# Kernel optimization log

Hardware: AMD Instinct MI355X
Metric: run time of the kernel (lower is better)

Reference implementation:

```python
import jax, jax.numpy as jnp
import numpy as np
import math

B, NX, NY = 8, 1024, 1024
DIM_X = DIM_Y = DIM = 1024
H = 8


def layer_norm(x, g, b, eps=1e-5):
    mu = jnp.mean(x, axis=-1, keepdims=True)
    var = jnp.mean(jnp.square(x - mu), axis=-1, keepdims=True)
    return (x - mu) * jax.lax.rsqrt(var + eps) * g + b


def setup_inputs() -> dict:
    key = jax.random.key(0)
    ks = jax.random.split(key, 12)
    s = 1.0 / math.sqrt(DIM)
    return {
        "X": jax.random.normal(ks[0], (B, NX, DIM_X), jnp.float32),
        "Y": jax.random.normal(ks[1], (B, NY, DIM_Y), jnp.float32),
        "mask": jax.random.bernoulli(ks[2], 0.1, (B, NY)),  # True = masked out
        "Wq": jax.random.normal(ks[3], (DIM_X, DIM), jnp.float32) * s,
        "bq": jnp.zeros((DIM,), jnp.float32),
        "Wk": jax.random.normal(ks[4], (DIM_Y, DIM), jnp.float32) * s,
        "bk": jnp.zeros((DIM,), jnp.float32),
        "Wv": jax.random.normal(ks[5], (DIM_Y, DIM), jnp.float32) * s,
        "bv": jnp.zeros((DIM,), jnp.float32),
        "Wo": jax.random.normal(ks[6], (DIM, DIM), jnp.float32) * s,
        "bo": jnp.zeros((DIM,), jnp.float32),
        "g1": jnp.ones((DIM,), jnp.float32),
        "b1": jnp.zeros((DIM,), jnp.float32),
        "g2": jnp.ones((DIM,), jnp.float32),
        "b2": jnp.zeros((DIM,), jnp.float32),
    }


def reference(X, Y, mask, Wq, bq, Wk, bk, Wv, bv, Wo, bo, g1, b1, g2, b2):
    Q = X @ Wq + bq            # [B, NX, DIM]
    K = Y @ Wk + bk            # [B, NY, DIM]
    V = Y @ Wv + bv            # [B, NY, DIM]
    Dh = DIM // H
    Qh = Q.reshape(B, NX, H, Dh)
    Kh = K.reshape(B, NY, H, Dh)
    Vh = V.reshape(B, NY, H, Dh)
    # NOTE: original scales by sqrt(dim) (full model dim), not sqrt(head_dim)
    logits = jnp.einsum("bqhd,bkhd->bhqk", Qh, Kh) / math.sqrt(DIM)
    logits = jnp.where(mask[:, None, None, :], -jnp.inf, logits)
    A = jax.nn.softmax(logits, axis=-1)
    A = jnp.where(jnp.isnan(A), 0.0, A)  # fully-masked rows -> 0
    attn = jnp.einsum("bhqk,bkhd->bqhd", A, Vh).reshape(B, NX, DIM)
    O = layer_norm(Q + attn, g1, b1)
    O = layer_norm(O + jax.nn.relu(O @ Wo + bo), g2, b2)
    return O
```

## Files before the change

### kernel.cpp

```cpp
#include <hip/hip_runtime.h>
#include <stdint.h>


typedef unsigned short u16;
typedef unsigned int u32;
typedef __attribute__((ext_vector_type(8))) short s16x8;
typedef __attribute__((ext_vector_type(4))) float f32x4;
typedef __attribute__((ext_vector_type(16))) float f32x16;
typedef __attribute__((ext_vector_type(4))) u16 u16x4;
typedef __attribute__((ext_vector_type(4))) u32 u32x4;

typedef __attribute__((address_space(1))) const void* as1cv;
typedef __attribute__((address_space(3))) void* as3v;

#define DEVINL __device__ __forceinline__

DEVINL u16 f2bf(float f) {
  union { float f; u32 u; } v; v.f = f;
  return (u16)((v.u + 0x7FFFu + ((v.u >> 16) & 1u)) >> 16);
}
DEVINL float bf2f(u16 x) {
  union { u32 u; float f; } v; v.u = ((u32)x) << 16;
  return v.f;
}
DEVINL u32 cvtpk_bf16(float lo, float hi) {
  u32 r;
  asm("v_cvt_pk_bf16_f32 %0, %1, %2" : "=v"(r) : "v"(lo), "v"(hi));
  return r;
}
DEVINL float fexp2(float x) {
  float r;
  asm("v_exp_f32 %0, %1" : "=v"(r) : "v"(x));
  return r;
}
DEVINL void gload_lds16(const void* g, void* l) {
  __builtin_amdgcn_global_load_lds((as1cv)g, (as3v)l, 16, 0, 0);
}
DEVINL f32x4 mfma16(s16x8 a, s16x8 b, f32x4 c) {
  return __builtin_amdgcn_mfma_f32_16x16x32_bf16(a, b, c, 0, 0, 0);
}
DEVINL f32x16 mfma32(s16x8 a, s16x8 b, f32x16 c) {
  return __builtin_amdgcn_mfma_f32_32x32x16_bf16(a, b, c, 0, 0, 0);
}
template <int N> DEVINL void wait_vm() {
  asm volatile("s_waitcnt vmcnt(%0)" :: "i"(N) : "memory");
  __builtin_amdgcn_sched_barrier(0);
}
DEVINL void wait_lgkm0() {
  asm volatile("s_waitcnt lgkmcnt(0)" ::: "memory");
  __builtin_amdgcn_sched_barrier(0);
}
DEVINL void barrier_raw() {
  __builtin_amdgcn_sched_barrier(0);
  __builtin_amdgcn_s_barrier();
  __builtin_amdgcn_sched_barrier(0);
}

__global__ __launch_bounds__(256) void prep_all(
    const float* __restrict__ X, u16* __restrict__ Xbf,
    const float* __restrict__ Y, u16* __restrict__ Ybf,
    const float* __restrict__ W0, const float* __restrict__ W1,
    const float* __restrict__ W2, const float* __restrict__ W3,
    u16* __restrict__ T0, u16* __restrict__ T1,
    u16* __restrict__ T2, u16* __restrict__ T3,
    const u32* __restrict__ mraw, float* __restrict__ maskb) {
  const int bid = blockIdx.x;
  const int t = threadIdx.x;
  if (bid < 2048) {
    const int base = bid * 256 + t;
#pragma unroll
    for (int k = 0; k < 4; ++k) {
      int e0 = (base + k * 524288) * 2;
      const float* in = X;
      u16* out = Xbf;
      if (e0 >= 2097152) { e0 -= 2097152; in = Y; out = Ybf; }
      float4 v0 = *(const float4*)(in + (size_t)e0 * 4);
      float4 v1 = *(const float4*)(in + (size_t)e0 * 4 + 4);
      u32x4 o;
      o[0] = cvtpk_bf16(v0.x, v0.y);
      o[1] = cvtpk_bf16(v0.z, v0.w);
      o[2] = cvtpk_bf16(v1.x, v1.y);
      o[3] = cvtpk_bf16(v1.z, v1.w);
      *(u32x4*)(out + (size_t)e0 * 4) = o;
    }
    return;
  }
  if (bid < 6144) {
    const int r = bid - 2048;
    const int z = r >> 10, tile = r & 1023;
    const int bx = tile & 31, by = tile >> 5;
    const float* W = (z == 0) ? W0 : (z == 1) ? W1 : (z == 2) ? W2 : W3;
    u16* T = (z == 0) ? T0 : (z == 1) ? T1 : (z == 2) ? T2 : T3;
    __shared__ float tl[32][33];
    const int tx = t & 31, ty = t >> 5;
    const int N0 = bx << 5, K0 = by << 5;
#pragma unroll
    for (int i = 0; i < 4; ++i)
      tl[ty + i * 8][tx] = W[(size_t)(K0 + ty + i * 8) * 1024 + N0 + tx];
    __syncthreads();
#pragma unroll
    for (int i = 0; i < 4; ++i)
      T[(size_t)(N0 + ty + i * 8) * 1024 + K0 + tx] = f2bf(tl[tx][ty + i * 8]);
    return;
  }
  __shared__ int mode;
  int fB = 0, fF = 0;
  for (int i = t; i < 2048; i += 256) {
    u32 v = mraw[i];
    if (v == 0x3F800000u) fF = 1;
    else if (v > 1u) fB = 1;
  }
  if (t == 0) mode = 0;
  __syncthreads();
  if (fB) atomicOr(&mode, 1);
  if (fF) atomicOr(&mode, 2);
  __syncthreads();
  const int md = mode;
  const int idx = (bid - 6144) * 256 + t;
  int v;
  if (md & 1)       v = ((const unsigned char*)mraw)[idx] != 0;
  else if (md & 2)  v = ((const float*)mraw)[idx] != 0.0f;
  else              v = ((const int*)mraw)[idx] != 0;
  maskb[idx] = v ? -3e30f : -11.54156032f;
}

#define GEMM_KLOOP                                                            \
  for (int kt = 0; kt < 16; ++kt) {                                           \
    s16x8 af0[4], bf0[4], af1[4], bf1[4];                                     \
    _Pragma("unroll")                                                         \
    for (int mi = 0; mi < 4; ++mi) {                                          \
      int row = wm * 64 + mi * 16 + lrow;                                     \
      int off = row * 128 + ((lk * 16) ^ ((row & 7) << 4));                   \
      af0[mi] = *(const s16x8*)((const char*)lA + off);                       \
    }                                                                         \
    _Pragma("unroll")                                                         \
    for (int ni = 0; ni < 4; ++ni) {                                          \
      int row = wn * 64 + ni * 16 + lrow;                                     \
      int off = row * 128 + ((lk * 16) ^ ((row & 7) << 4));                   \
      bf0[ni] = *(const s16x8*)((const char*)lB + off);                       \
    }                                                                         \
    _Pragma("unroll")                                                         \
    for (int mi = 0; mi < 4; ++mi)                                            \
      _Pragma("unroll")                                                       \
      for (int ni = 0; ni < 4; ++ni)                                          \
        acc[mi][ni] = mfma16(af0[mi], bf0[ni], acc[mi][ni]);                  \
    _Pragma("unroll")                                                         \
    for (int mi = 0; mi < 4; ++mi) {                                          \
      int row = wm * 64 + mi * 16 + lrow;                                     \
      int off = row * 128 + ((lk * 16 + 64) ^ ((row & 7) << 4));              \
      af1[mi] = *(const s16x8*)((const char*)lA + off);                       \
    }                                                                         \
    _Pragma("unroll")                                                         \
    for (int ni = 0; ni < 4; ++ni) {                                          \
      int row = wn * 64 + ni * 16 + lrow;                                     \
      int off = row * 128 + ((lk * 16 + 64) ^ ((row & 7) << 4));              \
      bf1[ni] = *(const s16x8*)((const char*)lB + off);                       \
    }                                                                         \
    wait_lgkm0();                                                             \
    barrier_raw();                                                            \
    if (kt < 15) {                                                            \
      const int kb = (kt + 1) * 128;                                          \
      _Pragma("unroll")                                                       \
      for (int c = 0; c < 4; ++c) {                                           \
        int row = (w * 4 + c) * 8 + sr;                                       \
        gload_lds16(gA + (size_t)row * 2048 + kb + scol,                      \
                    (char*)lA + (w * 4 + c) * 1024);                          \
        gload_lds16(gB + (size_t)row * 2048 + kb + scol,                      \
                    (char*)lB + (w * 4 + c) * 1024);                          \
      }                                                                       \
    }                                                                         \
    _Pragma("unroll")                                                         \
    for (int mi = 0; mi < 4; ++mi)                                            \
      _Pragma("unroll")                                                       \
      for (int ni = 0; ni < 4; ++ni)                                          \
        acc[mi][ni] = mfma16(af1[mi], bf1[ni], acc[mi][ni]);                  \
    __syncthreads();                                                          \
  }

#define GEMM_PROLOGUE                                                         \
  _Pragma("unroll")                                                           \
  for (int c = 0; c < 4; ++c) {                                               \
    int row = (w * 4 + c) * 8 + sr;                                           \
    gload_lds16(gA + (size_t)row * 2048 + scol, (char*)lA + (w * 4 + c) * 1024); \
    gload_lds16(gB + (size_t)row * 2048 + scol, (char*)lB + (w * 4 + c) * 1024); \
  }                                                                           \
  __syncthreads();

__global__ __launch_bounds__(256, 2) void gemm_qkv(
    const u16* __restrict__ Xbf, const u16* __restrict__ Ybf,
    const u16* __restrict__ Wqt, const u16* __restrict__ Wkt,
    const u16* __restrict__ Wvt,
    const float* __restrict__ bq, const float* __restrict__ bk,
    const float* __restrict__ bv,
    u16* __restrict__ Qbf, u16* __restrict__ Kbf, u16* __restrict__ Vt) {
  __shared__ u16 lA[128 * 64];
  __shared__ u16 lB[128 * 64];

  const int id = blockIdx.x;
  const int g = id >> 9;
  const int sub = id & 511;
  const int swz = (sub & 7) * 64 + (sub >> 3);
  const int mb = swz >> 3;
  const int nb = swz & 7;

  const u16* A    = (g == 0) ? Xbf : Ybf;
  const u16* Bt   = (g == 0) ? Wqt : (g == 1) ? Wkt : Wvt;
  const float* bias = (g == 0) ? bq : (g == 1) ? bk : bv;

  const int tid = threadIdx.x;
  const int w = tid >> 6, l = tid & 63;
  const int wm = w >> 1, wn = w & 1;
  const int lrow = l & 15, lk = l >> 4;
  const int sr = l >> 3;
  const int scol = ((l & 7) << 4) ^ (sr << 4);
  const char* gA = (const char*)A + (size_t)(mb * 128) * 2048;
  const char* gB = (const char*)Bt + (size_t)(nb * 128) * 2048;

  f32x4 acc[4][4];
#pragma unroll
  for (int i = 0; i < 4; ++i)
#pragma unroll
    for (int j = 0; j < 4; ++j) acc[i][j] = f32x4{0.f, 0.f, 0.f, 0.f};

  GEMM_PROLOGUE
  GEMM_KLOOP

  const int growb = mb * 128 + wm * 64;
  const int gcolb = nb * 128 + wn * 64;
  float bs[4];
#pragma unroll
  for (int ni = 0; ni < 4; ++ni) bs[ni] = bias[gcolb + ni * 16 + lrow];

  if (g == 2) {
#pragma unroll
    for (int mi = 0; mi < 4; ++mi) {
      const int grow0 = growb + mi * 16 + lk * 4;
#pragma unroll
      for (int ni = 0; ni < 4; ++ni) {
        const int gcol = gcolb + ni * 16 + lrow;
        u16x4 pk;
#pragma unroll
        for (int r = 0; r < 4; ++r) pk[r] = f2bf(acc[mi][ni][r] + bs[ni]);
        size_t flat = ((size_t)((grow0 >> 10) << 10) + gcol) * 1024 + (grow0 & 1023);
        *(u16x4*)(Vt + flat) = pk;
      }
    }
  } else {
    u16* outBF = g ? Kbf : Qbf;
#pragma unroll
    for (int mi = 0; mi < 4; ++mi) {
      const int grow0 = growb + mi * 16 + lk * 4;
#pragma unroll
      for (int ni = 0; ni < 4; ++ni) {
        const int gcol = gcolb + ni * 16 + lrow;
#pragma unroll
        for (int r = 0; r < 4; ++r)
          outBF[(size_t)(grow0 + r) * 1024 + gcol] = f2bf(acc[mi][ni][r] + bs[ni]);
      }
    }
  }
}

__global__ __launch_bounds__(256, 2) void gemm_o(
    const u16* __restrict__ A, const u16* __restrict__ Bt,
    const float* __restrict__ bias, u16* __restrict__ outBF,
    const u16* __restrict__ residBF) {
  __shared__ u16 lA[128 * 64];
  __shared__ u16 lB[128 * 64];

  const int id = blockIdx.x;
  const int swz = (id & 7) * 64 + (id >> 3);
  const int mb = swz >> 3;
  const int nb = swz & 7;

  const int tid = threadIdx.x;
  const int w = tid >> 6, l = tid & 63;
  const int wm = w >> 1, wn = w & 1;
  const int lrow = l & 15, lk = l >> 4;
  const int sr = l >> 3;
  const int scol = ((l & 7) << 4) ^ (sr << 4);
  const char* gA = (const char*)A + (size_t)(mb * 128) * 2048;
  const char* gB = (const char*)Bt + (size_t)(nb * 128) * 2048;

  f32x4 acc[4][4];
#pragma unroll
  for (int i = 0; i < 4; ++i)
#pragma unroll
    for (int j = 0; j < 4; ++j) acc[i][j] = f32x4{0.f, 0.f, 0.f, 0.f};

  GEMM_PROLOGUE
  GEMM_KLOOP

  const int growb = mb * 128 + wm * 64;
  const int gcolb = nb * 128 + wn * 64;
  float bs[4];
#pragma unroll
  for (int ni = 0; ni < 4; ++ni) bs[ni] = bias[gcolb + ni * 16 + lrow];

#pragma unroll
  for (int mi = 0; mi < 4; ++mi) {
    const int grow0 = growb + mi * 16 + lk * 4;
#pragma unroll
    for (int ni = 0; ni < 4; ++ni) {
      const int gcol = gcolb + ni * 16 + lrow;
#pragma unroll
      for (int r = 0; r < 4; ++r) {
        float v = acc[mi][ni][r] + bs[ni];
        size_t idx = (size_t)(grow0 + r) * 1024 + gcol;
        outBF[idx] = f2bf(bf2f(residBF[idx]) + fmaxf(v, 0.f));
      }
    }
  }
}

__global__ __launch_bounds__(256, 2) void attn_fwd(
    const u16* __restrict__ Qbf, const u16* __restrict__ Kbf,
    const u16* __restrict__ Vt, const float* __restrict__ maskb,
    u16* __restrict__ attnO) {
  __shared__ u16 lK[2][64 * 128];
  __shared__ u16 lV[128 * 64];
  __shared__ float lM[1024];

  const int id = blockIdx.x;
  const int xcd = id & 7, seq = id >> 3;
  const int bh = xcd * 8 + (seq >> 3);
  const int qb = seq & 7;
  const int b = bh >> 3, h = bh & 7;
  const int tid = threadIdx.x;
  const int w = tid >> 6, l = tid & 63;
  const int q32 = l & 31, hi = l >> 5;

  const u16* Qrow = Qbf + ((size_t)(b * 1024 + qb * 128 + w * 32 + q32)) * 1024 + h * 128;
  s16x8 qf[8];
#pragma unroll
  for (int dc = 0; dc < 8; ++dc) qf[dc] = *(const s16x8*)(Qrow + dc * 16 + hi * 8);

  const int srK = l >> 4, slK = l & 15;
  int soK[4], soV[4];
#pragma unroll
  for (int c = 0; c < 4; ++c) {
    int rowK = (w * 4 + c) * 4 + srK;
    soK[c] = rowK * 2048 + ((slK << 4) ^ ((rowK & 15) << 4));
    int pairid = (w * 4 + c) * 4 + (l >> 4);
    int u = (l & 15) ^ (pairid & 15);
    int d = pairid * 2 + (u >> 3);
    soV[c] = d * 2048 + (u & 7) * 16;
  }
  const char* pgK = (const char*)(Kbf + ((size_t)(b * 1024)) * 1024 + h * 128);
  const char* pgV = (const char*)(Vt + ((size_t)(b * 1024 + h * 128)) * 1024);

  const int bK = q32 * 256;
  const int swzK = (q32 & 15) << 4;
  const int hib = hi * 16;
  int loV[4];
#pragma unroll
  for (int c = 0; c < 4; ++c)
    loV[c] = (q32 >> 1) * 256 +
             (((((q32 & 1) << 3) | (c * 2 + hi)) ^ ((q32 >> 1) & 15)) << 4);

  if (w == 0) {
#pragma unroll
    for (int c = 0; c < 4; ++c)
      gload_lds16(maskb + b * 1024 + c * 256 + l * 4, (char*)lM + c * 1024);
  }
#pragma unroll
  for (int c = 0; c < 4; ++c)
    gload_lds16(pgK + soK[c], (char*)lK[0] + w * 4096 + c * 1024);

  float l_ = 0.f;
  f32x16 oacc[4];
#pragma unroll
  for (int i = 0; i < 4; ++i)
#pragma unroll
    for (int r = 0; r < 16; ++r) oacc[i][r] = 0.f;

  const float SCL = 0.04508422f;
  const char* pM0 = (const char*)lM + hi * 16;

#define STAGE_K(TN, BUF)                                                      \
  {                                                                           \
    const char* pk_ = pgK + (size_t)(TN)*131072;                              \
    _Pragma("unroll")                                                         \
    for (int c = 0; c < 4; ++c)                                               \
      gload_lds16(pk_ + soK[c], (char*)lK[BUF] + w * 4096 + c * 1024);        \
  }
#define STAGE_V(TN)                                                           \
  {                                                                           \
    const char* pv_ = pgV + (size_t)(TN)*128;                                 \
    _Pragma("unroll")                                                         \
    for (int c = 0; c < 4; ++c)                                               \
      gload_lds16(pv_ + soV[c], (char*)lV + w * 4096 + c * 1024);             \
  }

#define ATT_TILE(T, CUR, FIRST, LAST)                                         \
  {                                                                           \
    STAGE_V(T);                                                               \
    if (FIRST) { wait_vm<4>(); barrier_raw(); }                               \
    f32x16 sc[2];                                                             \
    _Pragma("unroll")                                                         \
    for (int kb = 0; kb < 2; ++kb)                                            \
      _Pragma("unroll")                                                       \
      for (int r = 0; r < 16; ++r) sc[kb][r] = 0.f;                           \
    __builtin_amdgcn_s_setprio(1);                                            \
    _Pragma("unroll")                                                         \
    for (int dc = 0; dc < 8; ++dc) {                                          \
      int offk = bK + (((dc * 32) | hib) ^ swzK);                             \
      _Pragma("unroll")                                                       \
      for (int kb = 0; kb < 2; ++kb) {                                        \
        s16x8 kf = *(const s16x8*)((const char*)lK[CUR] + offk + kb * 8192);  \
        sc[kb] = mfma32(kf, qf[dc], sc[kb]);                                  \
      }                                                                       \
    }                                                                         \
    __builtin_amdgcn_s_setprio(0);                                            \
    const char* pMa = pM0 + (T)*256;                                          \
    float rs = 0.f;                                                           \
    _Pragma("unroll")                                                         \
    for (int kb = 0; kb < 2; ++kb) {                                          \
      f32x4 mv[4];                                                            \
      _Pragma("unroll")                                                       \
      for (int g = 0; g < 4; ++g)                                             \
        mv[g] = *(const f32x4*)(pMa + kb * 128 + g * 32);                     \
      _Pragma("unroll")                                                       \
      for (int r = 0; r < 16; ++r) {                                          \
        float pe = fexp2(fmaf(sc[kb][r], SCL, mv[r >> 2][r & 3]));            \
        sc[kb][r] = pe;                                                       \
        rs += pe;                                                             \
      }                                                                       \
    }                                                                         \
    rs += __shfl_xor(rs, 32);                                                 \
    l_ += rs;                                                                 \
    if (!(LAST)) STAGE_K((T) + 1, (CUR) ^ 1);                                 \
    if (LAST) wait_vm<0>(); else wait_vm<4>();                                \
    barrier_raw();                                                            \
    _Pragma("unroll")                                                         \
    for (int kc = 0; kc < 4; ++kc) {                                          \
      const int kb = kc >> 1;                                                 \
      const int ra2 = (kc & 1) * 8;                                           \
      u32 x0 = cvtpk_bf16(sc[kb][ra2 + 0], sc[kb][ra2 + 1]);                  \
      u32 x1 = cvtpk_bf16(sc[kb][ra2 + 2], sc[kb][ra2 + 3]);                  \
      u32 y0 = cvtpk_bf16(sc[kb][ra2 + 4], sc[kb][ra2 + 5]);                  \
      u32 y1 = cvtpk_bf16(sc[kb][ra2 + 6], sc[kb][ra2 + 7]);                  \
      asm("v_permlane32_swap_b32 %0, %1" : "+v"(x0), "+v"(y0));               \
      asm("v_permlane32_swap_b32 %0, %1" : "+v"(x1), "+v"(y1));               \
      union { u32 u[4]; s16x8 v; } pa;                                        \
      pa.u[0] = x0; pa.u[1] = x1; pa.u[2] = y0; pa.u[3] = y1;                 \
      __builtin_amdgcn_s_setprio(1);                                          \
      _Pragma("unroll")                                                       \
      for (int nb = 0; nb < 4; ++nb) {                                        \
        s16x8 vb = *(const s16x8*)((const char*)lV + loV[kc] + nb * 4096);    \
        oacc[nb] = mfma32(pa.v, vb, oacc[nb]);                                \
      }                                                                       \
      __builtin_amdgcn_s_setprio(0);                                          \
    }                                                                         \
    if (!(LAST)) { wait_vm<0>(); barrier_raw(); }                             \
  }

  ATT_TILE(0, 0, true, false);
  for (int it = 0; it < 7; ++it) {
    ATT_TILE(2 * it + 1, 1, false, false);
    ATT_TILE(2 * it + 2, 0, false, false);
  }
  ATT_TILE(15, 1, false, true);
#undef ATT_TILE
#undef STAGE_K
#undef STAGE_V

  float inv = (l_ > 1e-20f) ? (1.0f / l_) : 0.f;
  u16* obase = attnO + ((size_t)(b * 1024 + qb * 128 + w * 32)) * 1024 + h * 128;
#pragma unroll
  for (int r = 0; r < 16; ++r) {
    int qr = (r & 3) + 8 * (r >> 2) + 4 * hi;
    float iv = __shfl(inv, qr);
#pragma unroll
    for (int nb = 0; nb < 4; ++nb)
      obase[(size_t)qr * 1024 + nb * 32 + q32] = f2bf(oacc[nb][r] * iv);
  }
}

__global__ __launch_bounds__(256) void ln_fused(
    const float* __restrict__ aF, const u16* __restrict__ aBF,
    const u16* __restrict__ baddBF, const float* __restrict__ g,
    const float* __restrict__ bt, float* __restrict__ outF,
    u16* __restrict__ outBF) {
  const int row = blockIdx.x;
  const int c = threadIdx.x << 2;
  const size_t base = (size_t)row * 1024 + c;
  float4 h;
  if (aF) {
    h = *(const float4*)(aF + base);
  } else {
    u16x4 u = *(const u16x4*)(aBF + base);
    h.x = bf2f(u[0]); h.y = bf2f(u[1]); h.z = bf2f(u[2]); h.w = bf2f(u[3]);
  }
  if (baddBF) {
    u16x4 u = *(const u16x4*)(baddBF + base);
    h.x += bf2f(u[0]); h.y += bf2f(u[1]); h.z += bf2f(u[2]); h.w += bf2f(u[3]);
  }
  float s = (h.x + h.y) + (h.z + h.w);
  float q = (h.x * h.x + h.y * h.y) + (h.z * h.z + h.w * h.w);
#pragma unroll
  for (int msk = 1; msk < 64; msk <<= 1) {
    s += __shfl_xor(s, msk);
    q += __shfl_xor(q, msk);
  }
  __shared__ float sh[8];
  const int w = threadIdx.x >> 6;
  if ((threadIdx.x & 63) == 0) { sh[w] = s; sh[4 + w] = q; }
  __syncthreads();
  s = (sh[0] + sh[1]) + (sh[2] + sh[3]);
  q = (sh[4] + sh[5]) + (sh[6] + sh[7]);
  const float mu = s * (1.f / 1024.f);
  const float var = q * (1.f / 1024.f) - mu * mu;
  const float rstd = rsqrtf(var + 1e-5f);
  const float4 gv = *(const float4*)(g + c);
  const float4 bv = *(const float4*)(bt + c);
  float4 o;
  o.x = (h.x - mu) * rstd * gv.x + bv.x;
  o.y = (h.y - mu) * rstd * gv.y + bv.y;
  o.z = (h.z - mu) * rstd * gv.z + bv.z;
  o.w = (h.w - mu) * rstd * gv.w + bv.w;
  if (outF) *(float4*)(outF + base) = o;
  if (outBF) {
    u16x4 ub; ub[0] = f2bf(o.x); ub[1] = f2bf(o.y); ub[2] = f2bf(o.z); ub[3] = f2bf(o.w);
    *(u16x4*)(outBF + base) = ub;
  }
}

extern "C" void kernel_launch(void* const* d_in, const int* in_sizes, int n_in,
                              void* d_out, int out_size, void* d_ws, size_t ws_size,
                              hipStream_t stream) {
  const float* X  = (const float*)d_in[0];
  const float* Y  = (const float*)d_in[1];
  const void*  mask = d_in[2];
  const float* Wq = (const float*)d_in[3];
  const float* bq = (const float*)d_in[4];
  const float* Wk = (const float*)d_in[5];
  const float* bk = (const float*)d_in[6];
  const float* Wv = (const float*)d_in[7];
  const float* bv = (const float*)d_in[8];
  const float* Wo = (const float*)d_in[9];
  const float* bo = (const float*)d_in[10];
  const float* g1 = (const float*)d_in[11];
  const float* b1 = (const float*)d_in[12];
  const float* g2 = (const float*)d_in[13];
  const float* b2 = (const float*)d_in[14];
  float* out = (float*)d_out;

  char* ws = (char*)d_ws;
  const size_t MB = 1024ull * 1024ull;
  u16* Xbf    = (u16*)(ws + 0);
  u16* Ybf    = (u16*)(ws + 16 * MB);
  u16* Qbf    = (u16*)(ws + 32 * MB);
  u16* Kbf    = (u16*)(ws + 48 * MB);
  u16* Vt     = (u16*)(ws + 64 * MB);
  u16* attnbf = (u16*)(ws + 80 * MB);
  u16* Wqt = (u16*)(ws + 112 * MB);
  u16* Wkt = (u16*)(ws + 114 * MB);
  u16* Wvt = (u16*)(ws + 116 * MB);
  u16* Wot = (u16*)(ws + 118 * MB);
  float* maskb = (float*)(ws + 120 * MB);
  u16* Rbf = Kbf;
  u16* O1bf = Xbf;

  prep_all<<<dim3(6176), dim3(256), 0, stream>>>(
      X, Xbf, Y, Ybf, Wq, Wk, Wv, Wo, Wqt, Wkt, Wvt, Wot,
      (const u32*)mask, maskb);

  gemm_qkv<<<dim3(1536), dim3(256), 0, stream>>>(
      Xbf, Ybf, Wqt, Wkt, Wvt, bq, bk, bv, Qbf, Kbf, Vt);

  attn_fwd<<<dim3(512), dim3(256), 0, stream>>>(Qbf, Kbf, Vt, maskb, attnbf);

  ln_fused<<<dim3(8192), dim3(256), 0, stream>>>(nullptr, Qbf, attnbf, g1, b1, nullptr, O1bf);
  gemm_o<<<dim3(512), dim3(256), 0, stream>>>(O1bf, Wot, bo, Rbf, O1bf);
  ln_fused<<<dim3(8192), dim3(256), 0, stream>>>(nullptr, Rbf, nullptr, g2, b2, out, nullptr);
}
```

Before: 169.8 us.

## Switch projection GEMMs to 256x128 tiles with 32x32x16 MFMA

Rewrites the QKV and output-projection GEMMs to use a 256x128 block tile (each wave computes 128x64) built from 32x32x16 bf16 MFMAs instead of 128x128 tiles of 16x16x32 MFMAs. It adds a new swizzled LDS layout and staging addresses, doubles LDS for A, and halves the grid sizes. The aim is more reuse per LDS fragment load and fewer blocks. In exchange there is more LDS per block and more accumulator registers, which may lower occupancy, and fewer blocks to balance across CUs.

```diff
diff --git a/kernel.cpp b/kernel.cpp
--- a/kernel.cpp
+++ b/kernel.cpp
@@ -35,9 +35,6 @@
 }
 DEVINL void gload_lds16(const void* g, void* l) {
   __builtin_amdgcn_global_load_lds((as1cv)g, (as3v)l, 16, 0, 0);
-}
-DEVINL f32x4 mfma16(s16x8 a, s16x8 b, f32x4 c) {
-  return __builtin_amdgcn_mfma_f32_16x16x32_bf16(a, b, c, 0, 0, 0);
 }
 DEVINL f32x16 mfma32(s16x8 a, s16x8 b, f32x16 c) {
   return __builtin_amdgcn_mfma_f32_32x32x16_bf16(a, b, c, 0, 0, 0);
@@ -124,67 +121,96 @@
   maskb[idx] = v ? -3e30f : -11.54156032f;
 }
 
-#define GEMM_KLOOP                                                            \
+#define G32_FRAG(LDSP, PV, CB)                                                \
+  (*(const s16x8*)((const char*)(LDSP) + (PV) * 256 +                         \
+                   (((CB)) ^ (((PV) & 15) << 4))))
+
+#define G32_SETUP                                                             \
+  const int tid = threadIdx.x;                                                \
+  const int w = tid >> 6, l = tid & 63;                                       \
+  const int wm = w >> 1, wn = w & 1;                                          \
+  const int q32 = l & 31, hi = l >> 5;                                        \
+  int soA[8], soB[4];                                                         \
+  _Pragma("unroll")                                                           \
+  for (int c = 0; c < 8; ++c) {                                               \
+    int P = (w * 8 + c) * 4 + (l >> 4);                                       \
+    int u = (l & 15) ^ (P & 15);                                              \
+    soA[c] = (2 * P + (u >> 3)) * 2048 + (u & 7) * 16;                        \
+  }                                                                           \
+  _Pragma("unroll")                                                           \
+  for (int c = 0; c < 4; ++c) {                                               \
+    int P = (w * 4 + c) * 4 + (l >> 4);                                       \
+    int u = (l & 15) ^ (P & 15);                                              \
+    soB[c] = (2 * P + (u >> 3)) * 2048 + (u & 7) * 16;                        \
+  }                                                                           \
+  int PA[4], PB[2];                                                           \
+  _Pragma("unroll")                                                           \
+  for (int mi = 0; mi < 4; ++mi) PA[mi] = wm * 64 + mi * 16 + (q32 >> 1);     \
+  _Pragma("unroll")                                                           \
+  for (int nj = 0; nj < 2; ++nj) PB[nj] = wn * 32 + nj * 16 + (q32 >> 1);     \
+  const int c0 = (q32 & 1) * 128 + hi * 16;                                   \
+  f32x16 acc[4][2];                                                           \
+  _Pragma("unroll")                                                           \
+  for (int i = 0; i < 4; ++i)                                                 \
+    _Pragma("unroll")                                                         \
+    for (int j = 0; j < 2; ++j)                                               \
+      _Pragma("unroll")                                                       \
+      for (int r = 0; r < 16; ++r) acc[i][j][r] = 0.f;
+
+#define G32_STAGE(KT)                                                         \
+  {                                                                           \
+    const char* pa_ = gA + (size_t)(KT)*128;                                  \
+    const char* pb_ = gB + (size_t)(KT)*128;                                  \
+    _Pragma("unroll")                                                         \
+    for (int c = 0; c < 8; ++c)                                               \
+      gload_lds16(pa_ + soA[c], (char*)lA + (w * 8 + c) * 1024);              \
+    _Pragma("unroll")                                                         \
+    for (int c = 0; c < 4; ++c)                                               \
+      gload_lds16(pb_ + soB[c], (char*)lB + (w * 4 + c) * 1024);              \
+  }
+
+#define G32_KLOOP                                                             \
+  G32_STAGE(0)                                                                \
+  __syncthreads();                                                            \
   for (int kt = 0; kt < 16; ++kt) {                                           \
-    s16x8 af0[4], bf0[4], af1[4], bf1[4];                                     \
-    _Pragma("unroll")                                                         \
-    for (int mi = 0; mi < 4; ++mi) {                                          \
-      int row = wm * 64 + mi * 16 + lrow;                                     \
-      int off = row * 128 + ((lk * 16) ^ ((row & 7) << 4));                   \
-      af0[mi] = *(const s16x8*)((const char*)lA + off);                       \
+    s16x8 af[4][2], bfg[2][2];                                                \
+    _Pragma("unroll")                                                         \
+    for (int ks = 0; ks < 2; ++ks) {                                          \
+      _Pragma("unroll")                                                       \
+      for (int mi = 0; mi < 4; ++mi)                                          \
+        af[mi][ks] = G32_FRAG(lA, PA[mi], c0 + ks * 32);                      \
+      _Pragma("unroll")                                                       \
+      for (int nj = 0; nj < 2; ++nj)                                          \
+        bfg[nj][ks] = G32_FRAG(lB, PB[nj], c0 + ks * 32);                     \
     }                                                                         \
     _Pragma("unroll")                                                         \
-    for (int ni = 0; ni < 4; ++ni) {                                          \
-      int row = wn * 64 + ni * 16 + lrow;                                     \
-      int off = row * 128 + ((lk * 16) ^ ((row & 7) << 4));                   \
-      bf0[ni] = *(const s16x8*)((const char*)lB + off);                       \
-    }                                                                         \
-    _Pragma("unroll")                                                         \
-    for (int mi = 0; mi < 4; ++mi)                                            \
-      _Pragma("unroll")                                                       \
-      for (int ni = 0; ni < 4; ++ni)                                          \
-        acc[mi][ni] = mfma16(af0[mi], bf0[ni], acc[mi][ni]);                  \
-    _Pragma("unroll")                                                         \
-    for (int mi = 0; mi < 4; ++mi) {                                          \
-      int row = wm * 64 + mi * 16 + lrow;                                     \
-      int off = row * 128 + ((lk * 16 + 64) ^ ((row & 7) << 4));              \
-      af1[mi] = *(const s16x8*)((const char*)lA + off);                       \
-    }                                                                         \
-    _Pragma("unroll")                                                         \
-    for (int ni = 0; ni < 4; ++ni) {                                          \
-      int row = wn * 64 + ni * 16 + lrow;                                     \
-      int off = row * 128 + ((lk * 16 + 64) ^ ((row & 7) << 4));              \
-      bf1[ni] = *(const s16x8*)((const char*)lB + off);                       \
+    for (int ks = 0; ks < 2; ++ks)                                            \
+      _Pragma("unroll")                                                       \
+      for (int mi = 0; mi < 4; ++mi)                                          \
+        _Pragma("unroll")                                                     \
+        for (int nj = 0; nj < 2; ++nj)                                        \
+          acc[mi][nj] = mfma32(af[mi][ks], bfg[nj][ks], acc[mi][nj]);         \
+    _Pragma("unroll")                                                         \
+    for (int ks = 0; ks < 2; ++ks) {                                          \
+      _Pragma("unroll")                                                       \
+      for (int mi = 0; mi < 4; ++mi)                                          \
+        af[mi][ks] = G32_FRAG(lA, PA[mi], c0 + 64 + ks * 32);                 \
+      _Pragma("unroll")                                                       \
+      for (int nj = 0; nj < 2; ++nj)                                          \
+        bfg[nj][ks] = G32_FRAG(lB, PB[nj], c0 + 64 + ks * 32);                \
     }                                                                         \
     wait_lgkm0();                                                             \
     barrier_raw();                                                            \
-    if (kt < 15) {                                                            \
-      const int kb = (kt + 1) * 128;                                          \
-      _Pragma("unroll")                                                       \
-      for (int c = 0; c < 4; ++c) {                                           \
-        int row = (w * 4 + c) * 8 + sr;                                       \
-        gload_lds16(gA + (size_t)row * 2048 + kb + scol,                      \
-                    (char*)lA + (w * 4 + c) * 1024);                          \
-        gload_lds16(gB + (size_t)row * 2048 + kb + scol,                      \
-                    (char*)lB + (w * 4 + c) * 1024);                          \
-      }                                                                       \
-    }                                                                         \
-    _Pragma("unroll")                                                         \
-    for (int mi = 0; mi < 4; ++mi)                                            \
-      _Pragma("unroll")                                                       \
-      for (int ni = 0; ni < 4; ++ni)                                          \
-        acc[mi][ni] = mfma16(af1[mi], bf1[ni], acc[mi][ni]);                  \
+    if (kt < 15) { G32_STAGE(kt + 1) }                                        \
+    _Pragma("unroll")                                                         \
+    for (int ks = 0; ks < 2; ++ks)                                            \
+      _Pragma("unroll")                                                       \
+      for (int mi = 0; mi < 4; ++mi)                                          \
+        _Pragma("unroll")                                                     \
+        for (int nj = 0; nj < 2; ++nj)                                        \
+          acc[mi][nj] = mfma32(af[mi][ks], bfg[nj][ks], acc[mi][nj]);         \
     __syncthreads();                                                          \
   }
-
-#define GEMM_PROLOGUE                                                         \
-  _Pragma("unroll")                                                           \
-  for (int c = 0; c < 4; ++c) {                                               \
-    int row = (w * 4 + c) * 8 + sr;                                           \
-    gload_lds16(gA + (size_t)row * 2048 + scol, (char*)lA + (w * 4 + c) * 1024); \
-    gload_lds16(gB + (size_t)row * 2048 + scol, (char*)lB + (w * 4 + c) * 1024); \
-  }                                                                           \
-  __syncthreads();
 
 __global__ __launch_bounds__(256, 2) void gemm_qkv(
     const u16* __restrict__ Xbf, const u16* __restrict__ Ybf,
@@ -193,13 +219,13 @@
     const float* __restrict__ bq, const float* __restrict__ bk,
     const float* __restrict__ bv,
     u16* __restrict__ Qbf, u16* __restrict__ Kbf, u16* __restrict__ Vt) {
-  __shared__ u16 lA[128 * 64];
-  __shared__ u16 lB[128 * 64];
+  __shared__ u16 lA[16384];
+  __shared__ u16 lB[8192];
 
   const int id = blockIdx.x;
-  const int g = id >> 9;
-  const int sub = id & 511;
-  const int swz = (sub & 7) * 64 + (sub >> 3);
+  const int g = id >> 8;
+  const int sub = id & 255;
+  const int swz = (sub & 7) * 32 + (sub >> 3);
   const int mb = swz >> 3;
   const int nb = swz & 7;
 
@@ -207,55 +233,48 @@
   const u16* Bt   = (g == 0) ? Wqt : (g == 1) ? Wkt : Wvt;
   const float* bias = (g == 0) ? bq : (g == 1) ? bk : bv;
 
-  const int tid = threadIdx.x;
-  const int w = tid >> 6, l = tid & 63;
-  const int wm = w >> 1, wn = w & 1;
-  const int lrow = l & 15, lk = l >> 4;
-  const int sr = l >> 3;
-  const int scol = ((l & 7) << 4) ^ (sr << 4);
-  const char* gA = (const char*)A + (size_t)(mb * 128) * 2048;
+  G32_SETUP
+  const char* gA = (const char*)A + (size_t)(mb * 256) * 2048;
   const char* gB = (const char*)Bt + (size_t)(nb * 128) * 2048;
 
-  f32x4 acc[4][4];
-#pragma unroll
-  for (int i = 0; i < 4; ++i)
-#pragma unroll
-    for (int j = 0; j < 4; ++j) acc[i][j] = f32x4{0.f, 0.f, 0.f, 0.f};
-
-  GEMM_PROLOGUE
-  GEMM_KLOOP
-
-  const int growb = mb * 128 + wm * 64;
+  G32_KLOOP
+
+  const int growb = mb * 256 + wm * 128;
   const int gcolb = nb * 128 + wn * 64;
-  float bs[4];
-#pragma unroll
-  for (int ni = 0; ni < 4; ++ni) bs[ni] = bias[gcolb + ni * 16 + lrow];
 
   if (g == 2) {
 #pragma unroll
-    for (int mi = 0; mi < 4; ++mi) {
-      const int grow0 = growb + mi * 16 + lk * 4;
-#pragma unroll
-      for (int ni = 0; ni < 4; ++ni) {
-        const int gcol = gcolb + ni * 16 + lrow;
-        u16x4 pk;
-#pragma unroll
-        for (int r = 0; r < 4; ++r) pk[r] = f2bf(acc[mi][ni][r] + bs[ni]);
-        size_t flat = ((size_t)((grow0 >> 10) << 10) + gcol) * 1024 + (grow0 & 1023);
-        *(u16x4*)(Vt + flat) = pk;
+    for (int nj = 0; nj < 2; ++nj) {
+      const int gcol = gcolb + nj * 32 + q32;
+      const float bsv = bias[gcol];
+#pragma unroll
+      for (int mi = 0; mi < 4; ++mi) {
+#pragma unroll
+        for (int rq = 0; rq < 4; ++rq) {
+          const int row0 = growb + mi * 32 + rq * 8 + hi * 4;
+          u16x4 pk;
+#pragma unroll
+          for (int i = 0; i < 4; ++i) pk[i] = f2bf(acc[mi][nj][rq * 4 + i] + bsv);
+          size_t flat = ((size_t)((row0 >> 10) << 10) + gcol) * 1024 + (row0 & 1023);
+          *(u16x4*)(Vt + flat) = pk;
+        }
       }
     }
   } else {
     u16* outBF = g ? Kbf : Qbf;
 #pragma unroll
-    for (int mi = 0; mi < 4; ++mi) {
-      const int grow0 = growb + mi * 16 + lk * 4;
-#pragma unroll
-      for (int ni = 0; ni < 4; ++ni) {
-        const int gcol = gcolb + ni * 16 + lrow;
-#pragma unroll
-        for (int r = 0; r < 4; ++r)
-          outBF[(size_t)(grow0 + r) * 1024 + gcol] = f2bf(acc[mi][ni][r] + bs[ni]);
+    for (int nj = 0; nj < 2; ++nj) {
+      const int gcol = gcolb + nj * 32 + q32;
+      const float bsv = bias[gcol];
+#pragma unroll
+      for (int mi = 0; mi < 4; ++mi) {
+#pragma unroll
+        for (int rq = 0; rq < 4; ++rq) {
+          const int row0 = growb + mi * 32 + rq * 8 + hi * 4;
+#pragma unroll
+          for (int i = 0; i < 4; ++i)
+            outBF[(size_t)(row0 + i) * 1024 + gcol] = f2bf(acc[mi][nj][rq * 4 + i] + bsv);
+        }
       }
     }
   }
@@ -265,49 +284,38 @@
     const u16* __restrict__ A, const u16* __restrict__ Bt,
     const float* __restrict__ bias, u16* __restrict__ outBF,
     const u16* __restrict__ residBF) {
-  __shared__ u16 lA[128 * 64];
-  __shared__ u16 lB[128 * 64];
+  __shared__ u16 lA[16384];
+  __shared__ u16 lB[8192];
 
   const int id = blockIdx.x;
-  const int swz = (id & 7) * 64 + (id >> 3);
+  const int swz = (id & 7) * 32 + (id >> 3);
   const int mb = swz >> 3;
   const int nb = swz & 7;
 
-  const int tid = threadIdx.x;
-  const int w = tid >> 6, l = tid & 63;
-  const int wm = w >> 1, wn = w & 1;
-  const int lrow = l & 15, lk = l >> 4;
-  const int sr = l >> 3;
-  const int scol = ((l & 7) << 4) ^ (sr << 4);
-  const char* gA = (const char*)A + (size_t)(mb * 128) * 2048;
+  G32_SETUP
+  const char* gA = (const char*)A + (size_t)(mb * 256) * 2048;
   const char* gB = (const char*)Bt + (size_t)(nb * 128) * 2048;
 
-  f32x4 acc[4][4];
-#pragma unroll
-  for (int i = 0; i < 4; ++i)
-#pragma unroll
-    for (int j = 0; j < 4; ++j) acc[i][j] = f32x4{0.f, 0.f, 0.f, 0.f};
-
-  GEMM_PROLOGUE
-  GEMM_KLOOP
-
-  const int growb = mb * 128 + wm * 64;
+  G32_KLOOP
+
+  const int growb = mb * 256 + wm * 128;
   const int gcolb = nb * 128 + wn * 64;
-  float bs[4];
-#pragma unroll
-  for (int ni = 0; ni < 4; ++ni) bs[ni] = bias[gcolb + ni * 16 + lrow];
-
-#pragma unroll
-  for (int mi = 0; mi < 4; ++mi) {
-    const int grow0 = growb + mi * 16 + lk * 4;
-#pragma unroll
-    for (int ni = 0; ni < 4; ++ni) {
-      const int gcol = gcolb + ni * 16 + lrow;
-#pragma unroll
-      for (int r = 0; r < 4; ++r) {
-        float v = acc[mi][ni][r] + bs[ni];
-        size_t idx = (size_t)(grow0 + r) * 1024 + gcol;
-        outBF[idx] = f2bf(bf2f(residBF[idx]) + fmaxf(v, 0.f));
+
+#pragma unroll
+  for (int nj = 0; nj < 2; ++nj) {
+    const int gcol = gcolb + nj * 32 + q32;
+    const float bsv = bias[gcol];
+#pragma unroll
+    for (int mi = 0; mi < 4; ++mi) {
+#pragma unroll
+      for (int rq = 0; rq < 4; ++rq) {
+        const int row0 = growb + mi * 32 + rq * 8 + hi * 4;
+#pragma unroll
+        for (int i = 0; i < 4; ++i) {
+          size_t idx = (size_t)(row0 + i) * 1024 + gcol;
+          outBF[idx] = f2bf(bf2f(residBF[idx]) +
+                            fmaxf(acc[mi][nj][rq * 4 + i] + bsv, 0.f));
+        }
       }
     }
   }
@@ -418,8 +426,8 @@
     for (int kb = 0; kb < 2; ++kb) {                                          \
       f32x4 mv[4];                                                            \
       _Pragma("unroll")                                                       \
-      for (int g = 0; g < 4; ++g)                                             \
-        mv[g] = *(const f32x4*)(pMa + kb * 128 + g * 32);                     \
+      for (int g2 = 0; g2 < 4; ++g2)                                          \
+        mv[g2] = *(const f32x4*)(pMa + kb * 128 + g2 * 32);                   \
       _Pragma("unroll")                                                       \
       for (int r = 0; r < 16; ++r) {                                          \
         float pe = fexp2(fmaf(sc[kb][r], SCL, mv[r >> 2][r & 3]));            \
@@ -566,12 +574,12 @@
       X, Xbf, Y, Ybf, Wq, Wk, Wv, Wo, Wqt, Wkt, Wvt, Wot,
       (const u32*)mask, maskb);
 
-  gemm_qkv<<<dim3(1536), dim3(256), 0, stream>>>(
+  gemm_qkv<<<dim3(768), dim3(256), 0, stream>>>(
       Xbf, Ybf, Wqt, Wkt, Wvt, bq, bk, bv, Qbf, Kbf, Vt);
 
   attn_fwd<<<dim3(512), dim3(256), 0, stream>>>(Qbf, Kbf, Vt, maskb, attnbf);
 
   ln_fused<<<dim3(8192), dim3(256), 0, stream>>>(nullptr, Qbf, attnbf, g1, b1, nullptr, O1bf);
-  gemm_o<<<dim3(512), dim3(256), 0, stream>>>(O1bf, Wot, bo, Rbf, O1bf);
+  gemm_o<<<dim3(256), dim3(256), 0, stream>>>(O1bf, Wot, bo, Rbf, O1bf);
   ln_fused<<<dim3(8192), dim3(256), 0, stream>>>(nullptr, Rbf, nullptr, g2, b2, out, nullptr);
 }
```

Result: slower. 186.6 us (+9.9%).
